# Optimization experiments

Measured on AMD Instinct MI355X. Metric: run time of the kernel, lower is better.

## Reference

```python
import jax, jax.numpy as jnp
import numpy as np
from jax import lax

B, N, C = 4, 16384, 384  # C = 2*dim
DIM = C // 2
HH = WW = 128


def setup_inputs() -> dict:
    key = jax.random.key(0)
    ks = jax.random.split(key, 5)
    x = jax.random.normal(ks[0], (B, N, C), dtype=jnp.float32)
    conv_w = jax.random.normal(ks[1], (DIM, DIM, 4, 4), dtype=jnp.float32) * (1.0 / np.sqrt(DIM * 16))
    conv_b = jax.random.normal(ks[2], (DIM,), dtype=jnp.float32) * 0.02
    ln_w = jnp.ones((C,), dtype=jnp.float32)
    ln_b = jnp.zeros((C,), dtype=jnp.float32)
    proj_w = jax.random.normal(ks[3], (C, C), dtype=jnp.float32) * (1.0 / np.sqrt(C))
    proj_b = jax.random.normal(ks[4], (C,), dtype=jnp.float32) * 0.02
    return {"x": x, "conv_w": conv_w, "conv_b": conv_b, "ln_w": ln_w,
            "ln_b": ln_b, "proj_w": proj_w, "proj_b": proj_b, "H": HH, "W": WW}


def _csb_forward(x, conv_w, conv_b, ln_w, ln_b, proj_w, proj_b, H, W):
    Bb, Nn, Cc = x.shape
    d = Cc // 2
    x1 = x[..., :d]   # [B, N, d]
    x2 = x[..., d:]   # [B, N, d]

    # --- SpatialCorrection ---
    img = jnp.transpose(x2, (0, 2, 1)).reshape(Bb, d, H, W)  # NCHW
    y = lax.conv_general_dilated(img, conv_w, window_strides=(4, 4),
                                 padding='VALID',
                                 dimension_numbers=('NCHW', 'OIHW', 'NCHW'))
    y = y + conv_b[None, :, None, None]
    x2c = y.reshape(Bb, d, Nn // 16)                          # [B, d, M]
    gate = jax.nn.sigmoid(jnp.einsum('bnd,bdm->bnm', x1, x2c))  # [B, N, M]
    sp = jnp.einsum('bnm,bdm->bnd', gate, x2c)                 # [B, N, d]

    # --- ChannelCorrection ---
    att = jax.nn.softmax(jnp.einsum('bnd,bne->bde', x1, x2), axis=-2)  # [B, d, d], softmax over dim=-2
    ch = jnp.einsum('bnd,bde->bne', x2, att)                   # [B, N, d]

    # --- concat + LN + proj ---
    cat = jnp.concatenate([sp, ch], axis=-1)                   # [B, N, 2d]
    mu = jnp.mean(cat, axis=-1, keepdims=True)
    var = jnp.mean(jnp.square(cat - mu), axis=-1, keepdims=True)
    ln = (cat - mu) * lax.rsqrt(var + 1e-5) * ln_w + ln_b
    out = jnp.einsum('bnc,oc->bno', ln, proj_w) + proj_b
    return jnp.transpose(out, (0, 2, 1))                       # [B, 2d, N]


def reference(x, conv_w, conv_b, ln_w, ln_b, proj_w, proj_b, H, W):
    return _csb_forward(x, conv_w, conv_b, ln_w, ln_b, proj_w, proj_b, H, W)
```

## Files before the change

kernel.cpp:

```cpp
#include <hip/hip_runtime.h>
#include <hip/hip_bf16.h>

#define BB 4
#define NN 16384
#define CC 384
#define DD 192
#define MM 1024

typedef __attribute__((ext_vector_type(8))) short short8;
typedef __attribute__((ext_vector_type(4))) float f32x4;
typedef unsigned short u16;

__device__ __forceinline__ float4 ld4(const float* p) { return *reinterpret_cast<const float4*>(p); }

__device__ __forceinline__ u16 bf16r(float f) {
    unsigned int u = __float_as_uint(f);
    return (u16)((u + 0x7FFFu + ((u >> 16) & 1u)) >> 16);
}
__device__ __forceinline__ unsigned int pk2(float a, float b) {
    return (unsigned int)bf16r(a) | ((unsigned int)bf16r(b) << 16);
}
__device__ __forceinline__ unsigned int pk2c(float a, float b) {
    __hip_bfloat162 h = __float22bfloat162_rn(make_float2(a, b));
    union { __hip_bfloat162 h2; unsigned int u; } c; c.h2 = h; return c.u;
}
__device__ __forceinline__ short8 as_s8(uint4 v) {
    union { uint4 u; short8 s; } x; x.u = v; return x.s;
}
__device__ __forceinline__ f32x4 mfma16(short8 a, short8 b, f32x4 c) {
    return __builtin_amdgcn_mfma_f32_16x16x32_bf16(a, b, c, 0, 0, 0);
}
__device__ __forceinline__ void gload16(const void* g, void* l) {
    __builtin_amdgcn_global_load_lds(
        (const __attribute__((address_space(1))) void*)g,
        (__attribute__((address_space(3))) void*)l, 16, 0, 0);
}

__global__ __launch_bounds__(256) void k_prep(const float* __restrict__ pw, u16* __restrict__ pwb)
{
    int i = blockIdx.x * 256 + threadIdx.x;
    float4 v = ld4(&pw[i * 4]);
    uint2 o; o.x = pk2(v.x, v.y); o.y = pk2(v.z, v.w);
    reinterpret_cast<uint2*>(pwb)[i] = o;
}

__global__ __launch_bounds__(256) void k_prepw(const float* __restrict__ cw, u16* __restrict__ cwb)
{
    int idx = blockIdx.x * 256 + threadIdx.x;
    int k8 = idx / 192, o = idx % 192;
    int px = k8 / 24;
    int i0 = (k8 % 24) * 8;
    float f[8];
    #pragma unroll
    for (int e = 0; e < 8; ++e) f[e] = cw[(size_t)(o * 192 + i0 + e) * 16 + px];
    uint4 v = make_uint4(pk2(f[0], f[1]), pk2(f[2], f[3]), pk2(f[4], f[5]), pk2(f[6], f[7]));
    reinterpret_cast<uint4*>(cwb)[idx] = v;
}

__global__ __launch_bounds__(256) void k_conv(const float* __restrict__ x,
                                              const u16* __restrict__ cwb,
                                              float* __restrict__ Cp2)
{
    const int bid = blockIdx.x;
    const int s = bid >> 8, pt = bid & 255;
    const int b = pt >> 6;
    const int m0 = (pt & 63) * 16;
    const int P0 = pt * 16;
    const int t = threadIdx.x;
    const int l = t & 63, w = t >> 6;
    const int l15 = l & 15, l4 = l >> 4;
    const int o0 = w * 48;

    const int m = m0 + l15;
    const int ph = m >> 5, pw_ = m & 31;
    const float* xp = x + ((size_t)(b * NN) + ph * 512 + pw_ * 4) * CC + DD;

    f32x4 acc[3];
    #pragma unroll
    for (int ft = 0; ft < 3; ++ft) acc[ft] = (f32x4){0.f, 0.f, 0.f, 0.f};

    for (int kt = 0; kt < 48; ++kt) {
        const int px = s * 8 + kt / 6;
        const int i0 = (kt % 6) * 32;
        const int kh = px >> 2, kw = px & 3;
        const float* src = xp + (size_t)(kh * 128 + kw) * CC + i0 + l4 * 8;
        float4 v0 = ld4(src), v1 = ld4(src + 4);
        short8 av = as_s8(make_uint4(pk2(v0.x, v0.y), pk2(v0.z, v0.w), pk2(v1.x, v1.y), pk2(v1.z, v1.w)));
        const int k8g = px * 24 + (kt % 6) * 4 + l4;
        #pragma unroll
        for (int ft = 0; ft < 3; ++ft) {
            int o = o0 + ft * 16 + l15;
            short8 bv = as_s8(*reinterpret_cast<const uint4*>(cwb + (size_t)(k8g * 192 + o) * 8));
            acc[ft] = mfma16(av, bv, acc[ft]);
        }
    }
    #pragma unroll
    for (int ft = 0; ft < 3; ++ft)
        #pragma unroll
        for (int i = 0; i < 4; ++i)
            Cp2[(size_t)(s * 4096 + P0 + l4 * 4 + i) * 192 + o0 + ft * 16 + l15] = acc[ft][i];
}

__global__ __launch_bounds__(256) void k_convred(const float* __restrict__ Cp2,
                                                 const float* __restrict__ cb,
                                                 u16* __restrict__ x2cT,
                                                 u16* __restrict__ x2cM)
{
    __shared__ u16 T[64 * 194];
    const int bid = blockIdx.x;
    const int b = bid >> 4, mc = bid & 15;
    const int P0 = b * 1024 + mc * 64;
    const int t = threadIdx.x;
    #pragma unroll
    for (int j = 0; j < 12; ++j) {
        int idx = j * 256 + t;
        int row = idx / 48, c4 = idx % 48;
        float4 v0 = ld4(&Cp2[(size_t)(P0 + row) * 192 + c4 * 4]);
        float4 v1 = ld4(&Cp2[(size_t)(4096 + P0 + row) * 192 + c4 * 4]);
        float4 bb = ld4(&cb[c4 * 4]);
        float r0 = v0.x + v1.x + bb.x, r1 = v0.y + v1.y + bb.y;
        float r2 = v0.z + v1.z + bb.z, r3 = v0.w + v1.w + bb.w;
        u16 h0 = bf16r(r0), h1 = bf16r(r1), h2 = bf16r(r2), h3 = bf16r(r3);
        uint2 ov; ov.x = (unsigned int)h0 | ((unsigned int)h1 << 16);
        ov.y = (unsigned int)h2 | ((unsigned int)h3 << 16);
        *reinterpret_cast<uint2*>(x2cT + (size_t)(P0 + row) * 192 + c4 * 4) = ov;
        T[row * 194 + c4 * 4 + 0] = h0; T[row * 194 + c4 * 4 + 1] = h1;
        T[row * 194 + c4 * 4 + 2] = h2; T[row * 194 + c4 * 4 + 3] = h3;
    }
    __syncthreads();
    #pragma unroll
    for (int j = 0; j < 6; ++j) {
        int u = j * 256 + t;
        int o = u >> 3, m8 = (u & 7) * 8;
        unsigned int pk[4];
        #pragma unroll
        for (int q = 0; q < 4; ++q) {
            u16 a = T[(m8 + q * 2) * 194 + o];
            u16 c = T[(m8 + q * 2 + 1) * 194 + o];
            pk[q] = (unsigned int)a | ((unsigned int)c << 16);
        }
        *reinterpret_cast<uint4*>(x2cM + ((size_t)(b * DD + o) * MM) + mc * 64 + m8) =
            make_uint4(pk[0], pk[1], pk[2], pk[3]);
    }
}

__global__ __launch_bounds__(512) void k_S(const float* __restrict__ x, float* __restrict__ Sp,
                                           int KS, int nkt)
{
    __shared__ char LS[384 * 128];
    const int bid = blockIdx.x;
    const int b = bid / KS, ks = bid % KS;
    const int n0 = ks * (NN / KS);
    const int t = threadIdx.x;
    const int l = t & 63, w = t >> 6;
    const int rg = w >> 2, cs = w & 3;
    const int l15 = l & 15, l4 = l >> 4, key = (l15 & 7) << 4;

    const int c0 = (t & 127) * 3;
    const int krow = t >> 7;

    f32x4 acc[6][3];
    #pragma unroll
    for (int dt = 0; dt < 6; ++dt)
        #pragma unroll
        for (int et = 0; et < 3; ++et) acc[dt][et] = (f32x4){0.f, 0.f, 0.f, 0.f};

    for (int kt = 0; kt < nkt; ++kt) {
        __syncthreads();
        #pragma unroll
        for (int i = 0; i < 8; ++i) {
            int k = i * 4 + krow;
            const float* src = &x[(size_t)(b * NN + n0 + kt * 32 + k) * CC + c0];
            #pragma unroll
            for (int j = 0; j < 3; ++j) {
                int c = c0 + j;
                float v = src[j];
                u16 hi = bf16r(v);
                float hif = __uint_as_float(((unsigned int)hi) << 16);
                u16 lo = bf16r(v - hif);
                int base = c * 128;
                int ck = (c & 7) << 4;
                *reinterpret_cast<u16*>(LS + base + ((k * 2) ^ ck)) = hi;
                *reinterpret_cast<u16*>(LS + base + ((64 + k * 2) ^ ck)) = lo;
            }
        }
        __syncthreads();
        short8 bf[3][2];
        #pragma unroll
        for (int et = 0; et < 3; ++et) {
            int c = 192 + cs * 48 + et * 16 + l15;
            #pragma unroll
            for (int hl = 0; hl < 2; ++hl)
                bf[et][hl] = *reinterpret_cast<const short8*>(LS + c * 128 + ((hl * 64 + l4 * 16) ^ key));
        }
        #pragma unroll
        for (int dt = 0; dt < 6; ++dt) {
            int c = rg * 96 + dt * 16 + l15;
            short8 ah = *reinterpret_cast<const short8*>(LS + c * 128 + ((l4 * 16) ^ key));
            short8 al = *reinterpret_cast<const short8*>(LS + c * 128 + ((64 + l4 * 16) ^ key));
            #pragma unroll
            for (int et = 0; et < 3; ++et) {
                acc[dt][et] = mfma16(ah, bf[et][0], acc[dt][et]);
                acc[dt][et] = mfma16(ah, bf[et][1], acc[dt][et]);
                acc[dt][et] = mfma16(al, bf[et][0], acc[dt][et]);
            }
        }
    }
    float* dst = Sp + (size_t)(ks * BB + b) * 36864;
    #pragma unroll
    for (int dt = 0; dt < 6; ++dt)
        #pragma unroll
        for (int et = 0; et < 3; ++et) {
            int e = cs * 48 + et * 16 + l15;
            #pragma unroll
            for (int i = 0; i < 4; ++i) {
                int d = rg * 96 + dt * 16 + l4 * 4 + i;
                dst[d * 192 + e] = acc[dt][et][i];
            }
        }
}

__global__ __launch_bounds__(256) void k_sreduce(const float* __restrict__ Sp, float* __restrict__ S, int KS)
{
    int idx = blockIdx.x * 256 + threadIdx.x;
    int b = idx / 36864, de = idx % 36864;
    float s = 0.f;
    for (int p = 0; p < KS; ++p) s += Sp[(size_t)(p * BB + b) * 36864 + de];
    S[(size_t)b * 36864 + de] = s;
}

__global__ __launch_bounds__(64) void k_softmax(const float* __restrict__ S, u16* __restrict__ attT)
{
    const int bid = blockIdx.x;
    const int b = bid / 192, e = bid % 192;
    const int l = threadIdx.x;
    const float* Sb = S + (size_t)b * 36864 + e;
    float v0 = Sb[(size_t)(l * 3 + 0) * 192];
    float v1 = Sb[(size_t)(l * 3 + 1) * 192];
    float v2 = Sb[(size_t)(l * 3 + 2) * 192];
    float m = fmaxf(fmaxf(v0, v1), v2);
    #pragma unroll
    for (int s = 1; s < 64; s <<= 1) m = fmaxf(m, __shfl_xor(m, s, 64));
    v0 = __expf(v0 - m); v1 = __expf(v1 - m); v2 = __expf(v2 - m);
    float sum = v0 + v1 + v2;
    #pragma unroll
    for (int s = 1; s < 64; s <<= 1) sum += __shfl_xor(sum, s, 64);
    float inv = __fdividef(1.f, sum);
    u16* dst = attT + (size_t)b * 36864 + (size_t)e * 192 + l * 3;
    dst[0] = bf16r(v0 * inv); dst[1] = bf16r(v1 * inv); dst[2] = bf16r(v2 * inv);
}

#define KF_PW  50176
#define KF_GT  73728

__global__ __launch_bounds__(512, 4) void k_fused2(
    const float* __restrict__ x, const u16* __restrict__ x2cT,
    const u16* __restrict__ attT,
    const float* __restrict__ lnw, const float* __restrict__ lnb,
    const u16* __restrict__ pwb, const float* __restrict__ pb,
    float* __restrict__ out)
{
    __shared__ alignas(16) char LB[77824];
    const int t = threadIdx.x;
    const int l = t & 63, w = t >> 6;
    const int rg = w >> 1, cs = w & 1;
    const int b = blockIdx.x >> 8;
    const int n0 = (blockIdx.x & 255) << 6;
    const int l15 = l & 15, l4 = l >> 4, key = (l15 & 7) << 4;
    const int key3 = (l15 & 3) << 4;
    const size_t xrow0 = (size_t)(b * NN + n0) * CC;
    const char* cbase = (const char*)x2cT;

    int goff[3], gmul[3];
    #pragma unroll
    for (int it = 0; it < 3; ++it) {
        int q = it * 8192 + w * 1024 + l * 16;
        if (q < 12288) {
            int m = q / 384, c = q % 384;
            goff[it] = b * 393216 + m * 384 + (c ^ ((m & 7) << 4));
            gmul[it] = 12288;
        } else {
            int qp = q - 12288;
            int r = qp >> 7, o = qp & 127;
            int op = o ^ ((r & 7) << 4);
            int d = r * 2 + (op >> 6);
            int m = (op & 63) >> 1;
            goff[it] = 1572864 + b * 393216 + d * 2048 + m * 2;
            gmul[it] = 64;
        }
    }

    short8 ax1[6];
    {
        int row = rg * 16 + l15;
        const float* src = &x[xrow0 + (size_t)row * CC + l4 * 8];
        #pragma unroll
        for (int k = 0; k < 6; ++k) {
            float4 v0 = ld4(src + k * 32), v1 = ld4(src + k * 32 + 4);
            ax1[k] = as_s8(make_uint4(pk2(v0.x, v0.y), pk2(v0.z, v0.w), pk2(v1.x, v1.y), pk2(v1.z, v1.w)));
        }
    }

    char* bA = LB;
    char* bB = LB + 24576;
    char* bC = LB + 49152;
    #pragma unroll
    for (int it = 0; it < 3; ++it)
        gload16(cbase + goff[it], bA + it * 8192 + w * 1024);
    #pragma unroll
    for (int it = 0; it < 3; ++it)
        gload16(cbase + goff[it] + gmul[it], bB + it * 8192 + w * 1024);

    f32x4 spa[6];
    #pragma unroll
    for (int nt = 0; nt < 6; ++nt) spa[nt] = (f32x4){0.f, 0.f, 0.f, 0.f};

    char* GTb = LB + KF_GT;

    for (int mc = 0; mc < 32; ++mc) {
        if (mc < 31) asm volatile("s_waitcnt vmcnt(3)" ::: "memory");
        else         asm volatile("s_waitcnt vmcnt(0)" ::: "memory");
        __builtin_amdgcn_s_barrier();
        __builtin_amdgcn_sched_barrier(0);
        if (mc + 2 < 32) {
            #pragma unroll
            for (int it = 0; it < 3; ++it)
                gload16(cbase + goff[it] + (mc + 2) * gmul[it], bC + it * 8192 + w * 1024);
        }
        const char* bufCT = bA;
        const char* bufCM = bA + 12288;

        f32x4 cp = (f32x4){0.f, 0.f, 0.f, 0.f};
        #pragma unroll
        for (int kblk = 0; kblk < 6; ++kblk) {
            short8 a_ = *reinterpret_cast<const short8*>(
                bufCT + (cs * 16 + l15) * 384 + ((kblk * 64 + l4 * 16) ^ key));
            cp = mfma16(a_, ax1[kblk], cp);
        }
        {
            float g0 = __fdividef(1.f, 1.f + __expf(-cp[0]));
            float g1 = __fdividef(1.f, 1.f + __expf(-cp[1]));
            float g2 = __fdividef(1.f, 1.f + __expf(-cp[2]));
            float g3 = __fdividef(1.f, 1.f + __expf(-cp[3]));
            uint2 gv; gv.x = pk2c(g0, g1); gv.y = pk2c(g2, g3);
            *reinterpret_cast<uint2*>(GTb + (rg * 16 + l15) * 64 +
                ((cs * 32 + l4 * 8) ^ key3)) = gv;
        }
        asm volatile("s_waitcnt lgkmcnt(0)" ::: "memory");
        __builtin_amdgcn_s_barrier();
        __builtin_amdgcn_sched_barrier(0);
        short8 ag = *reinterpret_cast<const short8*>(
            GTb + (rg * 16 + l15) * 64 + ((l4 * 16) ^ key3));
        #pragma unroll
        for (int nt = 0; nt < 6; ++nt) {
            const int d = cs * 96 + nt * 16 + l15;
            const int rr = d >> 1;
            short8 bv = *reinterpret_cast<const short8*>(
                bufCM + rr * 128 + ((((d & 1) * 64) + l4 * 16) ^ ((rr & 7) << 4)));
            spa[nt] = mfma16(ag, bv, spa[nt]);
        }
        char* tmp = bA; bA = bB; bB = bC; bC = tmp;
    }

    short8 ax2[6];
    {
        int row = rg * 16 + l15;
        const float* src = &x[xrow0 + (size_t)row * CC + DD + l4 * 8];
        #pragma unroll
        for (int k = 0; k < 6; ++k) {
            float4 v0 = ld4(src + k * 32), v1 = ld4(src + k * 32 + 4);
            ax2[k] = as_s8(make_uint4(pk2(v0.x, v0.y), pk2(v0.z, v0.w), pk2(v1.x, v1.y), pk2(v1.z, v1.w)));
        }
    }
    f32x4 cha[6];
    #pragma unroll
    for (int nt = 0; nt < 6; ++nt) cha[nt] = (f32x4){0.f, 0.f, 0.f, 0.f};
    const u16* atb = attT + (size_t)b * 36864;
    #pragma unroll
    for (int nt = 0; nt < 6; ++nt) {
        int e = cs * 96 + nt * 16 + l15;
        #pragma unroll
        for (int k = 0; k < 6; ++k) {
            short8 bv = *reinterpret_cast<const short8*>(atb + (size_t)e * 192 + k * 32 + l4 * 8);
            cha[nt] = mfma16(ax2[k], bv, cha[nt]);
        }
    }
    __syncthreads();

    #pragma unroll
    for (int nt = 0; nt < 6; ++nt) {
        int d = cs * 96 + nt * 16 + l15;
        #pragma unroll
        for (int i = 0; i < 4; ++i) {
            int row = rg * 16 + l4 * 4 + i;
            *reinterpret_cast<u16*>(LB + (row * 392 + d) * 2) = bf16r(spa[nt][i]);
            *reinterpret_cast<u16*>(LB + (row * 392 + DD + d) * 2) = bf16r(cha[nt][i]);
        }
    }
    __syncthreads();

    {
        const int rowL = t >> 3, q = t & 7;
        char* lbase = LB + rowL * 784 + q * 96;
        float s = 0.f, ss = 0.f;
        #pragma unroll
        for (int u = 0; u < 6; ++u) {
            uint4 pv = *reinterpret_cast<const uint4*>(lbase + u * 16);
            const unsigned int* pu = &pv.x;
            #pragma unroll
            for (int h = 0; h < 4; ++h) {
                float f0 = __uint_as_float(pu[h] << 16);
                float f1 = __uint_as_float(pu[h] & 0xFFFF0000u);
                s += f0 + f1; ss += f0 * f0 + f1 * f1;
            }
        }
        s += __shfl_xor(s, 1, 8);  s += __shfl_xor(s, 2, 8);  s += __shfl_xor(s, 4, 8);
        ss += __shfl_xor(ss, 1, 8); ss += __shfl_xor(ss, 2, 8); ss += __shfl_xor(ss, 4, 8);
        float mu = s * (1.f / 384.f);
        float var = ss * (1.f / 384.f) - mu * mu;
        float rs = rsqrtf(var + 1e-5f);
        const int c0 = q * 48;
        #pragma unroll
        for (int u = 0; u < 6; ++u) {
            uint4 pv = *reinterpret_cast<const uint4*>(lbase + u * 16);
            const unsigned int* pu = &pv.x;
            float4 w0 = ld4(&lnw[c0 + u * 8]), w1 = ld4(&lnw[c0 + u * 8 + 4]);
            float4 b0 = ld4(&lnb[c0 + u * 8]), b1 = ld4(&lnb[c0 + u * 8 + 4]);
            float f[8];
            #pragma unroll
            for (int h = 0; h < 4; ++h) {
                f[2 * h]     = __uint_as_float(pu[h] << 16);
                f[2 * h + 1] = __uint_as_float(pu[h] & 0xFFFF0000u);
            }
            f[0] = (f[0] - mu) * rs * w0.x + b0.x; f[1] = (f[1] - mu) * rs * w0.y + b0.y;
            f[2] = (f[2] - mu) * rs * w0.z + b0.z; f[3] = (f[3] - mu) * rs * w0.w + b0.w;
            f[4] = (f[4] - mu) * rs * w1.x + b1.x; f[5] = (f[5] - mu) * rs * w1.y + b1.y;
            f[6] = (f[6] - mu) * rs * w1.z + b1.z; f[7] = (f[7] - mu) * rs * w1.w + b1.w;
            *reinterpret_cast<uint4*>(lbase + u * 16) =
                make_uint4(pk2c(f[0], f[1]), pk2c(f[2], f[3]), pk2c(f[4], f[5]), pk2c(f[6], f[7]));
        }
    }

    f32x4 pacc[12];
    #pragma unroll
    for (int nt = 0; nt < 12; ++nt) pacc[nt] = (f32x4){0.f, 0.f, 0.f, 0.f};
    for (int kt = 0; kt < 12; ++kt) {
        __syncthreads();
        #pragma unroll
        for (int j = 0; j < 3; ++j) {
            int u = j * 512 + t;
            int o = u >> 2, c8 = (u & 3) * 8;
            uint4 pv = *reinterpret_cast<const uint4*>(pwb + (size_t)o * CC + kt * 32 + c8);
            *reinterpret_cast<uint4*>(LB + KF_PW + (((o * 32 + c8) * 2) ^ ((o & 7) << 4))) = pv;
        }
        __syncthreads();
        short8 av = *reinterpret_cast<const short8*>(
            LB + ((rg * 16 + l15) * 392 + kt * 32 + l4 * 8) * 2);
        #pragma unroll
        for (int nt = 0; nt < 12; ++nt) {
            int o = cs * 192 + nt * 16 + l15;
            short8 bv = *reinterpret_cast<const short8*>(
                LB + KF_PW + (((o * 32 + l4 * 8) * 2) ^ ((o & 7) << 4)));
            pacc[nt] = mfma16(av, bv, pacc[nt]);
        }
    }
    __syncthreads();

    float* T = reinterpret_cast<float*>(LB + KF_PW);
    for (int os = 0; os < 6; ++os) {
        if (cs == (os >= 3 ? 1 : 0)) {
            const int nt0 = (os % 3) * 4;
            #pragma unroll
            for (int nt = 0; nt < 4; ++nt) {
                int o_l = nt * 16 + l15;
                float bias = pb[os * 64 + o_l];
                #pragma unroll
                for (int i = 0; i < 4; ++i)
                    T[o_l * 68 + rg * 16 + l4 * 4 + i] = pacc[nt0 + nt][i] + bias;
            }
        }
        __syncthreads();
        {
            const int o_l = t >> 3, nq = t & 7;
            const size_t gbase = (size_t)(b * CC + os * 64 + o_l) * NN + n0 + nq * 8;
            float4 v0 = *reinterpret_cast<const float4*>(&T[o_l * 68 + nq * 8]);
            float4 v1 = *reinterpret_cast<const float4*>(&T[o_l * 68 + nq * 8 + 4]);
            *reinterpret_cast<float4*>(&out[gbase]) = v0;
            *reinterpret_cast<float4*>(&out[gbase + 4]) = v1;
        }
        __syncthreads();
    }
}

extern "C" void kernel_launch(void* const* d_in, const int* in_sizes, int n_in,
                              void* d_out, int out_size, void* d_ws, size_t ws_size,
                              hipStream_t stream)
{
    (void)in_sizes; (void)n_in; (void)out_size;
    const float* x   = (const float*)d_in[0];
    const float* cw  = (const float*)d_in[1];
    const float* cb  = (const float*)d_in[2];
    const float* lnw = (const float*)d_in[3];
    const float* lnb = (const float*)d_in[4];
    const float* pwm = (const float*)d_in[5];
    const float* pbv = (const float*)d_in[6];
    float* out = (float*)d_out;
    char* w0 = (char*)d_ws;

    u16* x2cT = (u16*)(w0);
    u16* x2cM = (u16*)(w0 + 1572864);
    u16* attT = (u16*)(w0 + 3145728);
    u16* pwb  = (u16*)(w0 + 3440640);
    u16* cwb  = (u16*)(w0 + 3735552);
    float* Cp2 = (float*)(w0 + 4915200);
    float* Sp  = (float*)(w0 + 11206656);
    float* Sf  = (float*)(w0 + 30081024);

    int KS = 32;
    if (ws_size >= (size_t)68419584) {
        KS = 64;
        Sp = (float*)(w0 + 30670848);
    }
    const int nkt = (NN / KS) / 32;

    hipLaunchKernelGGL(k_prep,    dim3(144),      dim3(256), 0, stream, pwm, pwb);
    hipLaunchKernelGGL(k_prepw,   dim3(288),      dim3(256), 0, stream, cw, cwb);
    hipLaunchKernelGGL(k_conv,    dim3(512),      dim3(256), 0, stream, x, cwb, Cp2);
    hipLaunchKernelGGL(k_convred, dim3(64),       dim3(256), 0, stream, Cp2, cb, x2cT, x2cM);
    hipLaunchKernelGGL(k_S,       dim3(BB * KS),  dim3(512), 0, stream, x, Sp, KS, nkt);
    hipLaunchKernelGGL(k_sreduce, dim3(576),      dim3(256), 0, stream, Sp, Sf, KS);
    hipLaunchKernelGGL(k_softmax, dim3(BB * 192), dim3(64),  0, stream, Sf, attT);
    hipLaunchKernelGGL(k_fused2,  dim3(1024),     dim3(512), 0, stream,
                       x, x2cT, attT, lnw, lnb, pwb, pbv, out);
}
```

Measured before the change: 276.7 us.

## Halve k_fused2 block size, giving each wave two 16-row tiles

k_fused2 now runs 256 threads per block instead of 512. Each wave processes two 16-row M tiles, so every B operand loaded from LDS (x2c chunks, attention matrix, projection weights) feeds two MFMAs and fewer LDS reads are needed per unit of work. Loop trip counts for staging loads, the LayerNorm pass and the output store are reworked to match the smaller block. The cost is roughly double the accumulator registers per wave, which may lower occupancy, and fewer waves per block to hide the per-chunk barrier latency.

```diff
diff --git a/kernel.cpp b/kernel.cpp
--- a/kernel.cpp
+++ b/kernel.cpp
@@ -253,7 +253,7 @@
 #define KF_PW  50176
 #define KF_GT  73728
 
-__global__ __launch_bounds__(512, 4) void k_fused2(
+__global__ __launch_bounds__(256, 2) void k_fused2(
     const float* __restrict__ x, const u16* __restrict__ x2cT,
     const u16* __restrict__ attT,
     const float* __restrict__ lnw, const float* __restrict__ lnb,
@@ -271,10 +271,10 @@
     const size_t xrow0 = (size_t)(b * NN + n0) * CC;
     const char* cbase = (const char*)x2cT;
 
-    int goff[3], gmul[3];
-    #pragma unroll
-    for (int it = 0; it < 3; ++it) {
-        int q = it * 8192 + w * 1024 + l * 16;
+    int goff[6], gmul[6];
+    #pragma unroll
+    for (int it = 0; it < 6; ++it) {
+        int q = it * 4096 + t * 16;
         if (q < 12288) {
             int m = q / 384, c = q % 384;
             goff[it] = b * 393216 + m * 384 + (c ^ ((m & 7) << 4));
@@ -290,14 +290,15 @@
         }
     }
 
-    short8 ax1[6];
-    {
-        int row = rg * 16 + l15;
+    short8 ax1[2][6];
+    #pragma unroll
+    for (int rt = 0; rt < 2; ++rt) {
+        int row = rg * 32 + rt * 16 + l15;
         const float* src = &x[xrow0 + (size_t)row * CC + l4 * 8];
         #pragma unroll
         for (int k = 0; k < 6; ++k) {
             float4 v0 = ld4(src + k * 32), v1 = ld4(src + k * 32 + 4);
-            ax1[k] = as_s8(make_uint4(pk2(v0.x, v0.y), pk2(v0.z, v0.w), pk2(v1.x, v1.y), pk2(v1.z, v1.w)));
+            ax1[rt][k] = as_s8(make_uint4(pk2(v0.x, v0.y), pk2(v0.z, v0.w), pk2(v1.x, v1.y), pk2(v1.z, v1.w)));
         }
     }
 
@@ -305,106 +306,127 @@
     char* bB = LB + 24576;
     char* bC = LB + 49152;
     #pragma unroll
-    for (int it = 0; it < 3; ++it)
-        gload16(cbase + goff[it], bA + it * 8192 + w * 1024);
-    #pragma unroll
-    for (int it = 0; it < 3; ++it)
-        gload16(cbase + goff[it] + gmul[it], bB + it * 8192 + w * 1024);
-
-    f32x4 spa[6];
-    #pragma unroll
-    for (int nt = 0; nt < 6; ++nt) spa[nt] = (f32x4){0.f, 0.f, 0.f, 0.f};
+    for (int it = 0; it < 6; ++it)
+        gload16(cbase + goff[it], bA + it * 4096 + w * 1024);
+    #pragma unroll
+    for (int it = 0; it < 6; ++it)
+        gload16(cbase + goff[it] + gmul[it], bB + it * 4096 + w * 1024);
+
+    f32x4 spa[2][6];
+    #pragma unroll
+    for (int rt = 0; rt < 2; ++rt)
+        #pragma unroll
+        for (int nt = 0; nt < 6; ++nt) spa[rt][nt] = (f32x4){0.f, 0.f, 0.f, 0.f};
 
     char* GTb = LB + KF_GT;
 
     for (int mc = 0; mc < 32; ++mc) {
-        if (mc < 31) asm volatile("s_waitcnt vmcnt(3)" ::: "memory");
+        if (mc < 31) asm volatile("s_waitcnt vmcnt(6)" ::: "memory");
         else         asm volatile("s_waitcnt vmcnt(0)" ::: "memory");
         __builtin_amdgcn_s_barrier();
         __builtin_amdgcn_sched_barrier(0);
         if (mc + 2 < 32) {
             #pragma unroll
-            for (int it = 0; it < 3; ++it)
-                gload16(cbase + goff[it] + (mc + 2) * gmul[it], bC + it * 8192 + w * 1024);
+            for (int it = 0; it < 6; ++it)
+                gload16(cbase + goff[it] + (mc + 2) * gmul[it], bC + it * 4096 + w * 1024);
         }
         const char* bufCT = bA;
         const char* bufCM = bA + 12288;
 
-        f32x4 cp = (f32x4){0.f, 0.f, 0.f, 0.f};
+        short8 bv[6];
+        #pragma unroll
+        for (int nt = 0; nt < 6; ++nt) {
+            const int d = cs * 96 + nt * 16 + l15;
+            const int rr = d >> 1;
+            bv[nt] = *reinterpret_cast<const short8*>(
+                bufCM + rr * 128 + ((((d & 1) * 64) + l4 * 16) ^ ((rr & 7) << 4)));
+        }
+
+        f32x4 cp[2];
+        cp[0] = (f32x4){0.f, 0.f, 0.f, 0.f};
+        cp[1] = (f32x4){0.f, 0.f, 0.f, 0.f};
         #pragma unroll
         for (int kblk = 0; kblk < 6; ++kblk) {
             short8 a_ = *reinterpret_cast<const short8*>(
                 bufCT + (cs * 16 + l15) * 384 + ((kblk * 64 + l4 * 16) ^ key));
-            cp = mfma16(a_, ax1[kblk], cp);
-        }
-        {
-            float g0 = __fdividef(1.f, 1.f + __expf(-cp[0]));
-            float g1 = __fdividef(1.f, 1.f + __expf(-cp[1]));
-            float g2 = __fdividef(1.f, 1.f + __expf(-cp[2]));
-            float g3 = __fdividef(1.f, 1.f + __expf(-cp[3]));
+            cp[0] = mfma16(a_, ax1[0][kblk], cp[0]);
+            cp[1] = mfma16(a_, ax1[1][kblk], cp[1]);
+        }
+        #pragma unroll
+        for (int rt = 0; rt < 2; ++rt) {
+            float g0 = __fdividef(1.f, 1.f + __expf(-cp[rt][0]));
+            float g1 = __fdividef(1.f, 1.f + __expf(-cp[rt][1]));
+            float g2 = __fdividef(1.f, 1.f + __expf(-cp[rt][2]));
+            float g3 = __fdividef(1.f, 1.f + __expf(-cp[rt][3]));
             uint2 gv; gv.x = pk2c(g0, g1); gv.y = pk2c(g2, g3);
-            *reinterpret_cast<uint2*>(GTb + (rg * 16 + l15) * 64 +
+            *reinterpret_cast<uint2*>(GTb + (rg * 32 + rt * 16 + l15) * 64 +
                 ((cs * 32 + l4 * 8) ^ key3)) = gv;
         }
         asm volatile("s_waitcnt lgkmcnt(0)" ::: "memory");
         __builtin_amdgcn_s_barrier();
         __builtin_amdgcn_sched_barrier(0);
-        short8 ag = *reinterpret_cast<const short8*>(
-            GTb + (rg * 16 + l15) * 64 + ((l4 * 16) ^ key3));
+        short8 ag[2];
+        #pragma unroll
+        for (int rt = 0; rt < 2; ++rt)
+            ag[rt] = *reinterpret_cast<const short8*>(
+                GTb + (rg * 32 + rt * 16 + l15) * 64 + ((l4 * 16) ^ key3));
         #pragma unroll
         for (int nt = 0; nt < 6; ++nt) {
-            const int d = cs * 96 + nt * 16 + l15;
-            const int rr = d >> 1;
-            short8 bv = *reinterpret_cast<const short8*>(
-                bufCM + rr * 128 + ((((d & 1) * 64) + l4 * 16) ^ ((rr & 7) << 4)));
-            spa[nt] = mfma16(ag, bv, spa[nt]);
+            spa[0][nt] = mfma16(ag[0], bv[nt], spa[0][nt]);
+            spa[1][nt] = mfma16(ag[1], bv[nt], spa[1][nt]);
         }
         char* tmp = bA; bA = bB; bB = bC; bC = tmp;
     }
 
-    short8 ax2[6];
-    {
-        int row = rg * 16 + l15;
+    short8 ax2[2][6];
+    #pragma unroll
+    for (int rt = 0; rt < 2; ++rt) {
+        int row = rg * 32 + rt * 16 + l15;
         const float* src = &x[xrow0 + (size_t)row * CC + DD + l4 * 8];
         #pragma unroll
         for (int k = 0; k < 6; ++k) {
             float4 v0 = ld4(src + k * 32), v1 = ld4(src + k * 32 + 4);
-            ax2[k] = as_s8(make_uint4(pk2(v0.x, v0.y), pk2(v0.z, v0.w), pk2(v1.x, v1.y), pk2(v1.z, v1.w)));
-        }
-    }
-    f32x4 cha[6];
-    #pragma unroll
-    for (int nt = 0; nt < 6; ++nt) cha[nt] = (f32x4){0.f, 0.f, 0.f, 0.f};
+            ax2[rt][k] = as_s8(make_uint4(pk2(v0.x, v0.y), pk2(v0.z, v0.w), pk2(v1.x, v1.y), pk2(v1.z, v1.w)));
+        }
+    }
+    f32x4 cha[2][6];
+    #pragma unroll
+    for (int rt = 0; rt < 2; ++rt)
+        #pragma unroll
+        for (int nt = 0; nt < 6; ++nt) cha[rt][nt] = (f32x4){0.f, 0.f, 0.f, 0.f};
     const u16* atb = attT + (size_t)b * 36864;
     #pragma unroll
     for (int nt = 0; nt < 6; ++nt) {
         int e = cs * 96 + nt * 16 + l15;
         #pragma unroll
         for (int k = 0; k < 6; ++k) {
-            short8 bv = *reinterpret_cast<const short8*>(atb + (size_t)e * 192 + k * 32 + l4 * 8);
-            cha[nt] = mfma16(ax2[k], bv, cha[nt]);
+            short8 bve = *reinterpret_cast<const short8*>(atb + (size_t)e * 192 + k * 32 + l4 * 8);
+            cha[0][nt] = mfma16(ax2[0][k], bve, cha[0][nt]);
+            cha[1][nt] = mfma16(ax2[1][k], bve, cha[1][nt]);
         }
     }
     __syncthreads();
 
     #pragma unroll
-    for (int nt = 0; nt < 6; ++nt) {
-        int d = cs * 96 + nt * 16 + l15;
-        #pragma unroll
-        for (int i = 0; i < 4; ++i) {
-            int row = rg * 16 + l4 * 4 + i;
-            *reinterpret_cast<u16*>(LB + (row * 392 + d) * 2) = bf16r(spa[nt][i]);
-            *reinterpret_cast<u16*>(LB + (row * 392 + DD + d) * 2) = bf16r(cha[nt][i]);
-        }
-    }
+    for (int rt = 0; rt < 2; ++rt)
+        #pragma unroll
+        for (int nt = 0; nt < 6; ++nt) {
+            int d = cs * 96 + nt * 16 + l15;
+            #pragma unroll
+            for (int i = 0; i < 4; ++i) {
+                int row = rg * 32 + rt * 16 + l4 * 4 + i;
+                *reinterpret_cast<u16*>(LB + (row * 392 + d) * 2) = bf16r(spa[rt][nt][i]);
+                *reinterpret_cast<u16*>(LB + (row * 392 + DD + d) * 2) = bf16r(cha[rt][nt][i]);
+            }
+        }
     __syncthreads();
 
     {
-        const int rowL = t >> 3, q = t & 7;
-        char* lbase = LB + rowL * 784 + q * 96;
+        const int rowL = t >> 2, q = t & 3;
+        char* lbase = LB + (rowL * 392 + q * 96) * 2;
         float s = 0.f, ss = 0.f;
         #pragma unroll
-        for (int u = 0; u < 6; ++u) {
+        for (int u = 0; u < 12; ++u) {
             uint4 pv = *reinterpret_cast<const uint4*>(lbase + u * 16);
             const unsigned int* pu = &pv.x;
             #pragma unroll
@@ -414,14 +436,14 @@
                 s += f0 + f1; ss += f0 * f0 + f1 * f1;
             }
         }
-        s += __shfl_xor(s, 1, 8);  s += __shfl_xor(s, 2, 8);  s += __shfl_xor(s, 4, 8);
-        ss += __shfl_xor(ss, 1, 8); ss += __shfl_xor(ss, 2, 8); ss += __shfl_xor(ss, 4, 8);
+        s += __shfl_xor(s, 1, 4);  s += __shfl_xor(s, 2, 4);
+        ss += __shfl_xor(ss, 1, 4); ss += __shfl_xor(ss, 2, 4);
         float mu = s * (1.f / 384.f);
         float var = ss * (1.f / 384.f) - mu * mu;
         float rs = rsqrtf(var + 1e-5f);
-        const int c0 = q * 48;
-        #pragma unroll
-        for (int u = 0; u < 6; ++u) {
+        const int c0 = q * 96;
+        #pragma unroll
+        for (int u = 0; u < 12; ++u) {
             uint4 pv = *reinterpret_cast<const uint4*>(lbase + u * 16);
             const unsigned int* pu = &pv.x;
             float4 w0 = ld4(&lnw[c0 + u * 8]), w1 = ld4(&lnw[c0 + u * 8 + 4]);
@@ -441,27 +463,34 @@
         }
     }
 
-    f32x4 pacc[12];
-    #pragma unroll
-    for (int nt = 0; nt < 12; ++nt) pacc[nt] = (f32x4){0.f, 0.f, 0.f, 0.f};
+    f32x4 pacc[2][12];
+    #pragma unroll
+    for (int rt = 0; rt < 2; ++rt)
+        #pragma unroll
+        for (int nt = 0; nt < 12; ++nt) pacc[rt][nt] = (f32x4){0.f, 0.f, 0.f, 0.f};
     for (int kt = 0; kt < 12; ++kt) {
         __syncthreads();
         #pragma unroll
-        for (int j = 0; j < 3; ++j) {
-            int u = j * 512 + t;
+        for (int j = 0; j < 6; ++j) {
+            int u = j * 256 + t;
             int o = u >> 2, c8 = (u & 3) * 8;
             uint4 pv = *reinterpret_cast<const uint4*>(pwb + (size_t)o * CC + kt * 32 + c8);
             *reinterpret_cast<uint4*>(LB + KF_PW + (((o * 32 + c8) * 2) ^ ((o & 7) << 4))) = pv;
         }
         __syncthreads();
-        short8 av = *reinterpret_cast<const short8*>(
-            LB + ((rg * 16 + l15) * 392 + kt * 32 + l4 * 8) * 2);
+        short8 av[2];
+        #pragma unroll
+        for (int rt = 0; rt < 2; ++rt) {
+            int row = rg * 32 + rt * 16 + l15;
+            av[rt] = *reinterpret_cast<const short8*>(LB + (row * 392 + kt * 32 + l4 * 8) * 2);
+        }
         #pragma unroll
         for (int nt = 0; nt < 12; ++nt) {
             int o = cs * 192 + nt * 16 + l15;
-            short8 bv = *reinterpret_cast<const short8*>(
+            short8 bvp = *reinterpret_cast<const short8*>(
                 LB + KF_PW + (((o * 32 + l4 * 8) * 2) ^ ((o & 7) << 4)));
-            pacc[nt] = mfma16(av, bv, pacc[nt]);
+            pacc[0][nt] = mfma16(av[0], bvp, pacc[0][nt]);
+            pacc[1][nt] = mfma16(av[1], bvp, pacc[1][nt]);
         }
     }
     __syncthreads();
@@ -475,18 +504,21 @@
                 int o_l = nt * 16 + l15;
                 float bias = pb[os * 64 + o_l];
                 #pragma unroll
-                for (int i = 0; i < 4; ++i)
-                    T[o_l * 68 + rg * 16 + l4 * 4 + i] = pacc[nt0 + nt][i] + bias;
+                for (int rt = 0; rt < 2; ++rt)
+                    #pragma unroll
+                    for (int i = 0; i < 4; ++i)
+                        T[o_l * 68 + rg * 32 + rt * 16 + l4 * 4 + i] = pacc[rt][nt0 + nt][i] + bias;
             }
         }
         __syncthreads();
         {
-            const int o_l = t >> 3, nq = t & 7;
-            const size_t gbase = (size_t)(b * CC + os * 64 + o_l) * NN + n0 + nq * 8;
-            float4 v0 = *reinterpret_cast<const float4*>(&T[o_l * 68 + nq * 8]);
-            float4 v1 = *reinterpret_cast<const float4*>(&T[o_l * 68 + nq * 8 + 4]);
-            *reinterpret_cast<float4*>(&out[gbase]) = v0;
-            *reinterpret_cast<float4*>(&out[gbase + 4]) = v1;
+            const int o_l = t >> 2, nq = t & 3;
+            const size_t gbase = (size_t)(b * CC + os * 64 + o_l) * NN + n0 + nq * 16;
+            #pragma unroll
+            for (int j = 0; j < 4; ++j) {
+                float4 v = *reinterpret_cast<const float4*>(&T[o_l * 68 + nq * 16 + j * 4]);
+                *reinterpret_cast<float4*>(&out[gbase + j * 4]) = v;
+            }
         }
         __syncthreads();
     }
@@ -530,6 +562,6 @@
     hipLaunchKernelGGL(k_S,       dim3(BB * KS),  dim3(512), 0, stream, x, Sp, KS, nkt);
     hipLaunchKernelGGL(k_sreduce, dim3(576),      dim3(256), 0, stream, Sp, Sf, KS);
     hipLaunchKernelGGL(k_softmax, dim3(BB * 192), dim3(64),  0, stream, Sf, attT);
-    hipLaunchKernelGGL(k_fused2,  dim3(1024),     dim3(512), 0, stream,
+    hipLaunchKernelGGL(k_fused2,  dim3(1024),     dim3(256), 0, stream,
                        x, x2cT, attT, lnw, lnb, pwb, pbv, out);
 }
```

Result: no change. 282.2 us (+2.0%).
